# Performance work log

Measured on AMD Instinct MI355X. Metric: run time of the kernel, lower is better.

The kernel has to match this reference:

```python
import jax, jax.numpy as jnp
import numpy as np

B, L, D = 8, 8192, 256
H = 4 * D
EPS_LN = 1e-5
EPS_RELU = 1e-6
MIN_A, MAX_A, OFFSET = 0, 3, 3


def setup_inputs() -> dict:
    key = jax.random.key(0)
    ks = jax.random.split(key, 6)
    def n(k, shape, s=0.02):
        return jax.random.normal(k, shape, jnp.float32) * s
    return {
        "x": jax.random.normal(ks[0], (B, L, D), jnp.float32),
        "g1": jnp.ones((D,), jnp.float32), "b1": jnp.zeros((D,), jnp.float32),
        "g2": jnp.ones((D,), jnp.float32), "b2": jnp.zeros((D,), jnp.float32),
        "filt_w": n(ks[1], (L, D)),
        "w1": n(ks[2], (D, H)), "bb1": jnp.zeros((H,), jnp.float32),
        "w2": n(ks[3], (H, D)), "bb2": jnp.zeros((D,), jnp.float32),
    }


def layernorm(x, g, b):
    m = jnp.mean(x, -1, keepdims=True)
    v = jnp.var(x, -1, keepdims=True)
    return (x - m) * jax.lax.rsqrt(v + EPS_LN) * g + b


def maxpool_same(x, w):
    # stride-1 max pool over the last (frequency) axis, SAME padding
    if w == 1:
        return x
    return jax.lax.reduce_window(x, -jnp.inf, jax.lax.max,
                                 (1, 1, w), (1, 1, 1), "SAME")


def spsd1d(xt):
    """SPSD1D: FFT-based multi-scale (alpha) max-pooling spectral filter.
    xt: (B, D, L). Keeps rfft bins that are local maxima at every scale
    2**alpha for alpha in [MIN_A, MAX_A]; the lowest OFFSET bins pass through.
    Returns filtered signal (B, D, L) and argmax-alpha holder (B, D, F)."""
    X = jnp.fft.rfft(xt, axis=-1)              # (B, D, F), F = L//2 + 1
    mag = jnp.abs(X)
    pooled = jnp.stack([maxpool_same(mag, 2 ** a)
                        for a in range(MIN_A, MAX_A + 1)], 0)  # (A, B, D, F)
    max_holder = jnp.argmax(pooled, axis=0)
    env = jnp.max(pooled, axis=0)
    keep = (mag >= env) | (jnp.arange(mag.shape[-1]) < OFFSET)
    Xf = jnp.where(keep, X, 0.0)
    out = jnp.fft.irfft(Xf, n=xt.shape[-1], axis=-1)
    return out, max_holder


def _block_forward(x, g1, b1, g2, b2, filt_w, w1, bb1, w2, bb2):
    # EpsilonReLU(LayerNorm(x))
    h = jax.nn.relu(layernorm(x, g1, b1)) + EPS_RELU      # (B, L, D)
    # GlobalSPSDFilter: spsd over sequence axis, then elementwise weight
    f, _max_holder = spsd1d(jnp.swapaxes(h, 1, 2))        # (B, D, L)
    x0 = jnp.swapaxes(f, 1, 2) * filt_w                   # (B, L, D)
    # MLP(LayerNorm(x0)); dropouts are identity in eval mode
    m = layernorm(x0, g2, b2)
    m = jax.nn.gelu(m @ w1 + bb1, approximate=False)
    x0 = m @ w2 + bb2
    return x + x0


def reference(x, g1, b1, g2, b2, filt_w, w1, bb1, w2, bb2):
    return _block_forward(x, g1, b1, g2, b2, filt_w, w1, bb1, w2, bb2)
```

## Files before the change

### kernel.cpp

```cpp
#include <hip/hip_runtime.h>
#include <hip/hip_bf16.h>

#define BSZ  8
#define LSEQ 8192
#define DDIM 256
#define HDIM 1024
#define MFFT 4096

typedef __bf16 bf16;
typedef __bf16 bf16x8 __attribute__((ext_vector_type(8)));
typedef __bf16 bf16x4 __attribute__((ext_vector_type(4)));
typedef float  f32x4  __attribute__((ext_vector_type(4)));

__device__ __forceinline__ void wave_reduce2(float& a, float& b) {
    #pragma unroll
    for (int off = 1; off < 64; off <<= 1) {
        a += __shfl_xor(a, off);
        b += __shfl_xor(b, off);
    }
}

__device__ __forceinline__ void gl_lds16(const void* g, void* l) {
    __builtin_amdgcn_global_load_lds(
        (const __attribute__((address_space(1))) unsigned int*)(unsigned long long)g,
        (__attribute__((address_space(3))) unsigned int*)(unsigned int)(unsigned long long)l,
        16, 0, 0);
}

__global__ __launch_bounds__(256) void k0_prep(const float* __restrict__ w1,
                                               const float* __restrict__ w2,
                                               bf16* __restrict__ w1t,
                                               bf16* __restrict__ w2ct,
                                               float2* __restrict__ tbl) {
    const int e = blockIdx.x * 256 + threadIdx.x;
    {
        const int h = e >> 8, d = e & 255;
        w1t[e] = (bf16)w1[d * HDIM + h];
    }
    {
        const int hh = e & 63, d = (e >> 6) & 255, c = e >> 14;
        w2ct[e] = (bf16)w2[(c * 64 + hh) * DDIM + d];
    }
    if (e <= 8184) {
        float ang;
        if (e < 3584) {
            const int f = e / 512 + 1, jj = e & 511;
            ang = -6.283185307179586f * (float)(f * jj) * (1.0f / 4096.0f);
        } else if (e < 4032) {
            const int t = e - 3584, f = t / 64 + 1, jj = t & 63;
            ang = -6.283185307179586f * (float)(f * jj) * (1.0f / 512.0f);
        } else if (e < 4088) {
            const int t = e - 4032, f = t / 8 + 1, jj = t & 7;
            ang = -6.283185307179586f * (float)(f * jj) * (1.0f / 64.0f);
        } else {
            const int k = e - 4088;
            ang = 3.14159265358979323846f * (float)k * (1.0f / 4096.0f);
        }
        tbl[e] = make_float2(cosf(ang), sinf(ang));
    }
}

__global__ __launch_bounds__(256) void k1_ln1_relu_T(const float* __restrict__ x,
                                                     const float* __restrict__ g1,
                                                     const float* __restrict__ b1,
                                                     float* __restrict__ ht) {
    __shared__ float tile[DDIM][33];
    const int tid  = threadIdx.x;
    const int wave = tid >> 6, lane = tid & 63;
    const int b  = blockIdx.x >> 8;
    const int l0 = (blockIdx.x & 255) << 5;
    const float4 g4 = *(const float4*)&g1[lane * 4];
    const float4 b4 = *(const float4*)&b1[lane * 4];
    for (int r8 = 0; r8 < 8; ++r8) {
        const int l = r8 * 4 + wave;
        const float4 v = *(const float4*)&x[(b * LSEQ + l0 + l) * DDIM + lane * 4];
        float s = v.x + v.y + v.z + v.w;
        float q = v.x * v.x + v.y * v.y + v.z * v.z + v.w * v.w;
        wave_reduce2(s, q);
        const float mean = s * (1.0f / 256.0f);
        const float var  = q * (1.0f / 256.0f) - mean * mean;
        const float rstd = rsqrtf(var + 1e-5f);
        const float vv[4] = {v.x, v.y, v.z, v.w};
        const float gg[4] = {g4.x, g4.y, g4.z, g4.w};
        const float bb[4] = {b4.x, b4.y, b4.z, b4.w};
        #pragma unroll
        for (int j = 0; j < 4; ++j) {
            float t = (vv[j] - mean) * rstd * gg[j] + bb[j];
            t = fmaxf(t, 0.0f) + 1e-6f;
            tile[lane * 4 + j][l] = t;
        }
    }
    __syncthreads();
    for (int i = tid; i < DDIM * 32; i += 256) {
        const int d = i >> 5, ll = i & 31;
        ht[(b * DDIM + d) * LSEQ + l0 + ll] = tile[d][ll];
    }
}

__device__ __forceinline__ int zs(int p) { return p ^ ((p >> 4) & 15); }
__device__ __forceinline__ float2 cmulf(float2 a, float2 b) {
    return make_float2(fmaf(a.x, b.x, -a.y * b.y), fmaf(a.x, b.y, a.y * b.x));
}
__device__ __forceinline__ float2 f2add(float2 a, float2 b) { return make_float2(a.x + b.x, a.y + b.y); }
__device__ __forceinline__ float2 f2sub(float2 a, float2 b) { return make_float2(a.x - b.x, a.y - b.y); }
#define CSQ2 0.70710678118654752440f

__device__ __forceinline__ void dft8(float2 a0, float2 a1, float2 a2, float2 a3,
                                     float2 a4, float2 a5, float2 a6, float2 a7,
                                     float2& y0, float2& y1, float2& y2, float2& y3,
                                     float2& y4, float2& y5, float2& y6, float2& y7) {
    const float2 s0 = f2add(a0, a4), s1 = f2add(a1, a5), s2 = f2add(a2, a6), s3 = f2add(a3, a7);
    const float2 d0 = f2sub(a0, a4), d1 = f2sub(a1, a5), d2 = f2sub(a2, a6), d3 = f2sub(a3, a7);
    const float2 d1t = make_float2(CSQ2 * (d1.x + d1.y), CSQ2 * (d1.y - d1.x));
    const float2 d2t = make_float2(d2.y, -d2.x);
    const float2 d3t = make_float2(CSQ2 * (d3.y - d3.x), -CSQ2 * (d3.x + d3.y));
    const float2 u0 = f2add(s0, s2), u1 = f2add(s1, s3);
    const float2 v0 = f2sub(s0, s2);
    const float2 sd = f2sub(s1, s3);
    const float2 v1 = make_float2(sd.y, -sd.x);
    const float2 e0 = f2add(d0, d2t), e1 = f2add(d1t, d3t);
    const float2 f0 = f2sub(d0, d2t);
    const float2 dd = f2sub(d1t, d3t);
    const float2 f1 = make_float2(dd.y, -dd.x);
    y0 = f2add(u0, u1); y4 = f2sub(u0, u1);
    y2 = f2add(v0, v1); y6 = f2sub(v0, v1);
    y1 = f2add(e0, e1); y5 = f2sub(e0, e1);
    y3 = f2add(f0, f1); y7 = f2sub(f0, f1);
}

template<int LQ, int TOFF>
__device__ __forceinline__ void stage8(float2* Z, const float2* __restrict__ tw, int tid) {
    const int q = 1 << LQ;
    const int j = tid & (q - 1);
    const int base = ((tid >> LQ) << (LQ + 3)) + j;
    const float2 a0 = Z[zs(base)],         a1 = Z[zs(base + q)];
    const float2 a2 = Z[zs(base + 2 * q)], a3 = Z[zs(base + 3 * q)];
    const float2 a4 = Z[zs(base + 4 * q)], a5 = Z[zs(base + 5 * q)];
    const float2 a6 = Z[zs(base + 6 * q)], a7 = Z[zs(base + 7 * q)];
    float2 y0, y1, y2, y3, y4, y5, y6, y7;
    dft8(a0, a1, a2, a3, a4, a5, a6, a7, y0, y1, y2, y3, y4, y5, y6, y7);
    y1 = cmulf(y1, tw[TOFF + j]);
    y2 = cmulf(y2, tw[TOFF + q + j]);
    y3 = cmulf(y3, tw[TOFF + 2 * q + j]);
    y4 = cmulf(y4, tw[TOFF + 3 * q + j]);
    y5 = cmulf(y5, tw[TOFF + 4 * q + j]);
    y6 = cmulf(y6, tw[TOFF + 5 * q + j]);
    y7 = cmulf(y7, tw[TOFF + 6 * q + j]);
    Z[zs(base)]         = y0;
    Z[zs(base + 4 * q)] = y1;
    Z[zs(base + 2 * q)] = y2;
    Z[zs(base + 6 * q)] = y3;
    Z[zs(base + q)]     = y4;
    Z[zs(base + 5 * q)] = y5;
    Z[zs(base + 3 * q)] = y6;
    Z[zs(base + 7 * q)] = y7;
    __syncthreads();
}

__device__ __forceinline__ void stage8_last(float2* Z, int tid) {
    const int base = tid << 3;
    const float2 a0 = Z[zs(base)],     a1 = Z[zs(base + 1)];
    const float2 a2 = Z[zs(base + 2)], a3 = Z[zs(base + 3)];
    const float2 a4 = Z[zs(base + 4)], a5 = Z[zs(base + 5)];
    const float2 a6 = Z[zs(base + 6)], a7 = Z[zs(base + 7)];
    __syncthreads();
    float2 y0, y1, y2, y3, y4, y5, y6, y7;
    dft8(a0, a1, a2, a3, a4, a5, a6, a7, y0, y1, y2, y3, y4, y5, y6, y7);
    const int r9 = (int)(__brev((unsigned)tid) >> 23);
    Z[zs(r9)]        = y0;
    Z[zs(512 + r9)]  = y1;
    Z[zs(1024 + r9)] = y2;
    Z[zs(1536 + r9)] = y3;
    Z[zs(2048 + r9)] = y4;
    Z[zs(2560 + r9)] = y5;
    Z[zs(3072 + r9)] = y6;
    Z[zs(3584 + r9)] = y7;
    __syncthreads();
}

__device__ __forceinline__ void fft4096(float2* Z, const float2* __restrict__ tw, int tid) {
    stage8<9, 0>(Z, tw, tid);
    stage8<6, 3584>(Z, tw, tid);
    stage8<3, 4032>(Z, tw, tid);
    stage8_last(Z, tid);
}

__global__ __launch_bounds__(512, 4) void k2_spsd(float* __restrict__ ht,
                                                  const float2* __restrict__ tw) {
    __shared__ float2 Z[MFFT];
    __shared__ float  mg[MFFT + 1];
    const int tid = threadIdx.x;
    float* row = ht + (size_t)blockIdx.x * LSEQ;
    const float2* U = tw + 4088;

    for (int m = tid; m < MFFT; m += 512)
        Z[zs(m)] = *(const float2*)&row[2 * m];
    __syncthreads();

    fft4096(Z, tw, tid);

    for (int k = tid; k <= MFFT; k += 512) {
        const int ka = k & (MFFT - 1);
        const int kb = (MFFT - k) & (MFFT - 1);
        const float2 A = Z[zs(ka)], Bc = Z[zs(kb)];
        const float zex = 0.5f * (A.x + Bc.x), zey = 0.5f * (A.y - Bc.y);
        const float zox = 0.5f * (A.y + Bc.y), zoy = -0.5f * (A.x - Bc.x);
        const float2 u = U[k];
        const float cs = u.x, sn = -u.y;
        const float xr = zex + zox * cs - zoy * sn;
        const float xi = zey + zox * sn + zoy * cs;
        mg[k] = sqrtf(xr * xr + xi * xi);
    }
    __syncthreads();

    for (int k = tid; k <= 2048; k += 512) {
        const int km = (MFFT - k) & (MFFT - 1);
        const float2 Pk = Z[zs(k)];
        const float2 Pm = Z[zs(km)];
        const float2 u = U[k];
        const float cs = u.x, sn = u.y;
        const float zex = 0.5f * (Pk.x + Pm.x), zey = 0.5f * (Pk.y - Pm.y);
        const float zox = 0.5f * (Pk.y + Pm.y), zoy = -0.5f * (Pk.x - Pm.x);
        float xkr = zex + zox * cs + zoy * sn;
        float xki = zey - zox * sn + zoy * cs;
        const float zex2 = 0.5f * (Pm.x + Pk.x), zey2 = 0.5f * (Pm.y - Pk.y);
        const float zox2 = 0.5f * (Pm.y + Pk.y), zoy2 = -0.5f * (Pm.x - Pk.x);
        float xmr = zex2 - zox2 * cs + zoy2 * sn;
        float xmi = zey2 - zox2 * sn - zoy2 * cs;
        const int jm = MFFT - k;
        bool keepk, keepm;
        {
            const int lo = (k - 3 < 0) ? 0 : k - 3;
            const int hi = (k + 4 > 4096) ? 4096 : k + 4;
            float mx = mg[k];
            for (int t2 = lo; t2 <= hi; ++t2) mx = fmaxf(mx, mg[t2]);
            keepk = (k < 3) || (mg[k] >= mx);
        }
        {
            const int hi = (jm + 4 > 4096) ? 4096 : jm + 4;
            float mx = mg[jm];
            for (int t2 = jm - 3; t2 <= hi; ++t2) mx = fmaxf(mx, mg[t2]);
            keepm = (mg[jm] >= mx);
        }
        if (!keepk) { xkr = 0.0f; xki = 0.0f; }
        if (!keepm) { xmr = 0.0f; xmi = 0.0f; }
        const float zpex = 0.5f * (xkr + xmr), zpey = 0.5f * (xki - xmi);
        const float dfx  = 0.5f * (xkr - xmr), dfy  = 0.5f * (xki + xmi);
        const float zpox = dfx * cs - dfy * sn, zpoy = dfx * sn + dfy * cs;
        const float2 zk = make_float2(zpex - zpoy, zpey + zpox);
        const float zex3 = 0.5f * (xmr + xkr), zey3 = 0.5f * (xmi - xki);
        const float df2x = 0.5f * (xmr - xkr), df2y = 0.5f * (xmi + xki);
        const float zo3x = -df2x * cs - df2y * sn, zo3y = df2x * sn - df2y * cs;
        const float2 zm = make_float2(zex3 - zo3y, zey3 + zo3x);
        Z[zs(k)] = make_float2(zk.x, -zk.y);
        if (k != 0 && k != 2048) Z[zs(MFFT - k)] = make_float2(zm.x, -zm.y);
    }
    __syncthreads();

    fft4096(Z, tw, tid);

    const float invM = 1.0f / (float)MFFT;
    for (int m = tid; m < MFFT; m += 512) {
        const float2 z = Z[zs(m)];
        *(float2*)&row[2 * m] = make_float2(z.x * invM, -z.y * invM);
    }
}

__global__ __launch_bounds__(256) void k3_filt_ln2(const float* __restrict__ ht,
                                                   const float* __restrict__ fw,
                                                   const float* __restrict__ g2,
                                                   const float* __restrict__ b2,
                                                   bf16* __restrict__ aln) {
    __shared__ float tile[DDIM][33];
    const int tid  = threadIdx.x;
    const int wave = tid >> 6, lane = tid & 63;
    const int b  = blockIdx.x >> 8;
    const int l0 = (blockIdx.x & 255) << 5;
    for (int i = tid; i < DDIM * 32; i += 256) {
        const int d = i >> 5, ll = i & 31;
        tile[d][ll] = ht[(b * DDIM + d) * LSEQ + l0 + ll];
    }
    __syncthreads();
    const float4 g4 = *(const float4*)&g2[lane * 4];
    const float4 bb4 = *(const float4*)&b2[lane * 4];
    for (int r8 = 0; r8 < 8; ++r8) {
        const int l = r8 * 4 + wave;
        const int gl = l0 + l;
        const float4 f4 = *(const float4*)&fw[gl * DDIM + lane * 4];
        float v[4];
        v[0] = tile[lane * 4 + 0][l] * f4.x;
        v[1] = tile[lane * 4 + 1][l] * f4.y;
        v[2] = tile[lane * 4 + 2][l] * f4.z;
        v[3] = tile[lane * 4 + 3][l] * f4.w;
        float s = v[0] + v[1] + v[2] + v[3];
        float q = v[0] * v[0] + v[1] * v[1] + v[2] * v[2] + v[3] * v[3];
        wave_reduce2(s, q);
        const float mean = s * (1.0f / 256.0f);
        const float var  = q * (1.0f / 256.0f) - mean * mean;
        const float rstd = rsqrtf(var + 1e-5f);
        const float gg[4] = {g4.x, g4.y, g4.z, g4.w};
        const float bb[4] = {bb4.x, bb4.y, bb4.z, bb4.w};
        bf16x4 o;
        #pragma unroll
        for (int j = 0; j < 4; ++j)
            o[j] = (bf16)((v[j] - mean) * rstd * gg[j] + bb[j]);
        *(bf16x4*)&aln[(b * LSEQ + gl) * DDIM + lane * 4] = o;
    }
}

#define LDS_W1 0
#define LDS_W2 32768
#define LDS_LM 65536
#define LDS_TOT 81920

__global__ __launch_bounds__(512, 2) void k4_mlp(const bf16* __restrict__ aln,
                                                 const bf16* __restrict__ w1t,
                                                 const bf16* __restrict__ w2ct,
                                                 const float* __restrict__ bb1,
                                                 const float* __restrict__ bb2,
                                                 const float* __restrict__ x,
                                                 float* __restrict__ out) {
    extern __shared__ char sm[];
    const int tid = threadIdx.x;
    const int lane = tid & 63, w = tid >> 6;
    const int rowLane = lane & 15, grp = lane >> 4;
    const int wm = w >> 1, wn = w & 1;
    const int row0 = blockIdx.x << 7;
    const int sw = (rowLane & 7) << 4;

    bf16x8 aF[2][8];
    #pragma unroll
    for (int fm = 0; fm < 2; ++fm) {
        const size_t rb = (size_t)(row0 + wm * 32 + fm * 16 + rowLane) * DDIM;
        #pragma unroll
        for (int ks = 0; ks < 8; ++ks)
            aF[fm][ks] = *(const bf16x8*)(aln + rb + ks * 32 + grp * 8);
    }
    {
        const char* g1 = (const char*)w1t;
        #pragma unroll
        for (int r = 0; r < 4; ++r) {
            const int o = r * 8192 + tid * 16;
            gl_lds16(g1 + (o ^ (((o >> 9) & 7) << 4)), sm + LDS_W1 + o);
        }
    }
    __syncthreads();

    f32x4 acc[2][8];
    #pragma unroll
    for (int i = 0; i < 2; ++i)
        #pragma unroll
        for (int j2 = 0; j2 < 8; ++j2) acc[i][j2] = (f32x4){0.f, 0.f, 0.f, 0.f};

    for (int c = 0; c < 16; ++c) {
        {
            const char* g2 = (const char*)(w2ct + (size_t)c * DDIM * 64);
            #pragma unroll
            for (int r = 0; r < 4; ++r) {
                const int o = r * 8192 + tid * 16;
                gl_lds16(g2 + (o ^ (((o >> 7) & 7) << 4)), sm + LDS_W2 + o);
            }
        }
        const float bias0 = bb1[c * 64 + wn * 32 + rowLane];
        const float bias1 = bb1[c * 64 + wn * 32 + 16 + rowLane];

        f32x4 p00 = {0.f,0.f,0.f,0.f}, p01 = p00, p10 = p00, p11 = p00;
        const int hc0 = wn * 32 + rowLane;
        #pragma unroll
        for (int ks = 0; ks < 8; ++ks) {
            const int kb = (ks * 64 + grp * 16) ^ sw;
            const bf16x8 b0 = *(const bf16x8*)(sm + LDS_W1 + hc0 * 512 + kb);
            const bf16x8 b1 = *(const bf16x8*)(sm + LDS_W1 + (hc0 + 16) * 512 + kb);
            p00 = __builtin_amdgcn_mfma_f32_16x16x32_bf16(aF[0][ks], b0, p00, 0, 0, 0);
            p10 = __builtin_amdgcn_mfma_f32_16x16x32_bf16(aF[1][ks], b0, p10, 0, 0, 0);
            p01 = __builtin_amdgcn_mfma_f32_16x16x32_bf16(aF[0][ks], b1, p01, 0, 0, 0);
            p11 = __builtin_amdgcn_mfma_f32_16x16x32_bf16(aF[1][ks], b1, p11, 0, 0, 0);
        }
        #pragma unroll
        for (int fm = 0; fm < 2; ++fm)
        #pragma unroll
        for (int fn = 0; fn < 2; ++fn) {
            const f32x4 pv = fm ? (fn ? p11 : p10) : (fn ? p01 : p00);
            const int pcol2 = (wn * 32 + fn * 16 + rowLane) * 2;
            const float bias = fn ? bias1 : bias0;
            #pragma unroll
            for (int j = 0; j < 4; ++j) {
                const int prow = wm * 32 + fm * 16 + grp * 4 + j;
                const float v = pv[j] + bias;
                const float ge = 0.5f * v * (1.0f + erff(v * 0.70710678118654752f));
                *(bf16*)(sm + LDS_LM + prow * 128 + (pcol2 ^ ((prow & 7) << 4))) = (bf16)ge;
            }
        }
        __syncthreads();
        if (c < 15) {
            const char* g1 = (const char*)(w1t + (size_t)(c + 1) * 64 * DDIM);
            #pragma unroll
            for (int r = 0; r < 4; ++r) {
                const int o = r * 8192 + tid * 16;
                gl_lds16(g1 + (o ^ (((o >> 9) & 7) << 4)), sm + LDS_W1 + o);
            }
        }
        const int ar0 = wm * 32 + rowLane;
        #pragma unroll
        for (int kk = 0; kk < 2; ++kk) {
            const int kb = (kk * 64 + grp * 16) ^ sw;
            const bf16x8 a0 = *(const bf16x8*)(sm + LDS_LM + ar0 * 128 + kb);
            const bf16x8 a1 = *(const bf16x8*)(sm + LDS_LM + (ar0 + 16) * 128 + kb);
            #pragma unroll
            for (int fn = 0; fn < 8; ++fn) {
                const int dcol = wn * 128 + fn * 16 + rowLane;
                const bf16x8 bw = *(const bf16x8*)(sm + LDS_W2 + dcol * 128 + kb);
                acc[0][fn] = __builtin_amdgcn_mfma_f32_16x16x32_bf16(a0, bw, acc[0][fn], 0, 0, 0);
                acc[1][fn] = __builtin_amdgcn_mfma_f32_16x16x32_bf16(a1, bw, acc[1][fn], 0, 0, 0);
            }
        }
        __syncthreads();
    }
    #pragma unroll
    for (int fn = 0; fn < 8; ++fn) {
        const int dcol = wn * 128 + fn * 16 + rowLane;
        const float b2v = bb2[dcol];
        #pragma unroll
        for (int fm = 0; fm < 2; ++fm)
        #pragma unroll
        for (int j = 0; j < 4; ++j) {
            const int orow = row0 + wm * 32 + fm * 16 + grp * 4 + j;
            const int gi = orow * DDIM + dcol;
            out[gi] = acc[fm][fn][j] + b2v + x[gi];
        }
    }
}

extern "C" void kernel_launch(void* const* d_in, const int* in_sizes, int n_in,
                              void* d_out, int out_size, void* d_ws, size_t ws_size,
                              hipStream_t stream) {
    (void)in_sizes; (void)n_in; (void)out_size; (void)ws_size;
    const float* x   = (const float*)d_in[0];
    const float* g1  = (const float*)d_in[1];
    const float* b1  = (const float*)d_in[2];
    const float* g2  = (const float*)d_in[3];
    const float* b2  = (const float*)d_in[4];
    const float* fw  = (const float*)d_in[5];
    const float* w1  = (const float*)d_in[6];
    const float* bb1 = (const float*)d_in[7];
    const float* w2  = (const float*)d_in[8];
    const float* bb2 = (const float*)d_in[9];
    float* out = (float*)d_out;
    char*  ws  = (char*)d_ws;

    bf16*   aln  = (bf16*)ws;
    bf16*   w1t  = (bf16*)(ws + (size_t)33554432);
    bf16*   w2ct = (bf16*)(ws + (size_t)34078720);
    float2* tbl  = (float2*)(ws + (size_t)34603008);
    float* ht = out;

    k0_prep<<<dim3(1024), dim3(256), 0, stream>>>(w1, w2, w1t, w2ct, tbl);
    k1_ln1_relu_T<<<dim3(2048), dim3(256), 0, stream>>>(x, g1, b1, ht);
    k2_spsd<<<dim3(2048), dim3(512), 0, stream>>>(ht, tbl);
    k3_filt_ln2<<<dim3(2048), dim3(256), 0, stream>>>(ht, fw, g2, b2, aln);
    k4_mlp<<<dim3(512), dim3(512), LDS_TOT, stream>>>(aln, w1t, w2ct, bb1, bb2, x, out);
}
```

Baseline: 256.9 us.

## Pre-pack MLP weights in MFMA fragment order and halve hidden chunk size

The prep kernel now writes W1 and W2 in bf16 laid out in MFMA fragment order, so the MLP kernel can copy weights into LDS contiguously and read them without XOR swizzling. The hidden-dimension chunk shrinks from 64 to 32, which halves LDS use to 40 KB per block and allows more blocks per CU. The cost is twice as many loop iterations, and so twice as many barriers and more per-chunk overhead, with fewer MFMAs issued between each sync.

New measurement: 259.1 us. Within noise of the previous version (+0.8%).

```diff
diff --git a/kernel.cpp b/kernel.cpp
--- a/kernel.cpp
+++ b/kernel.cpp
@@ -29,17 +29,19 @@
 
 __global__ __launch_bounds__(256) void k0_prep(const float* __restrict__ w1,
                                                const float* __restrict__ w2,
-                                               bf16* __restrict__ w1t,
-                                               bf16* __restrict__ w2ct,
+                                               bf16* __restrict__ w1k,
+                                               bf16* __restrict__ w2k,
                                                float2* __restrict__ tbl) {
     const int e = blockIdx.x * 256 + threadIdx.x;
     {
-        const int h = e >> 8, d = e & 255;
-        w1t[e] = (bf16)w1[d * HDIM + h];
+        const int c = e >> 13, r = e & 8191;
+        const int ks = r >> 10, grp = (r >> 8) & 3, hh = (r >> 3) & 31, j = r & 7;
+        w1k[e] = (bf16)w1[(ks * 32 + grp * 8 + j) * HDIM + c * 32 + hh];
     }
     {
-        const int hh = e & 63, d = (e >> 6) & 255, c = e >> 14;
-        w2ct[e] = (bf16)w2[(c * 64 + hh) * DDIM + d];
+        const int c = e >> 13, r = e & 8191;
+        const int grp = r >> 11, d = (r >> 3) & 255, j = r & 7;
+        w2k[e] = (bf16)w2[(c * 32 + grp * 8 + j) * DDIM + d];
     }
     if (e <= 8184) {
         float ang;
@@ -309,13 +311,13 @@
 }
 
 #define LDS_W1 0
-#define LDS_W2 32768
-#define LDS_LM 65536
-#define LDS_TOT 81920
+#define LDS_W2 16384
+#define LDS_LM 32768
+#define LDS_TOT 40960
 
 __global__ __launch_bounds__(512, 2) void k4_mlp(const bf16* __restrict__ aln,
-                                                 const bf16* __restrict__ w1t,
-                                                 const bf16* __restrict__ w2ct,
+                                                 const bf16* __restrict__ w1k,
+                                                 const bf16* __restrict__ w2k,
                                                  const float* __restrict__ bb1,
                                                  const float* __restrict__ bb2,
                                                  const float* __restrict__ x,
@@ -326,7 +328,6 @@
     const int rowLane = lane & 15, grp = lane >> 4;
     const int wm = w >> 1, wn = w & 1;
     const int row0 = blockIdx.x << 7;
-    const int sw = (rowLane & 7) << 4;
 
     bf16x8 aF[2][8];
     #pragma unroll
@@ -337,12 +338,9 @@
             aF[fm][ks] = *(const bf16x8*)(aln + rb + ks * 32 + grp * 8);
     }
     {
-        const char* g1 = (const char*)w1t;
-        #pragma unroll
-        for (int r = 0; r < 4; ++r) {
-            const int o = r * 8192 + tid * 16;
-            gl_lds16(g1 + (o ^ (((o >> 9) & 7) << 4)), sm + LDS_W1 + o);
-        }
+        const char* g1 = (const char*)w1k;
+        gl_lds16(g1 + tid * 16, sm + LDS_W1 + tid * 16);
+        gl_lds16(g1 + 8192 + tid * 16, sm + LDS_W1 + 8192 + tid * 16);
     }
     __syncthreads();
 
@@ -352,67 +350,50 @@
         #pragma unroll
         for (int j2 = 0; j2 < 8; ++j2) acc[i][j2] = (f32x4){0.f, 0.f, 0.f, 0.f};
 
-    for (int c = 0; c < 16; ++c) {
+    for (int c = 0; c < 32; ++c) {
         {
-            const char* g2 = (const char*)(w2ct + (size_t)c * DDIM * 64);
-            #pragma unroll
-            for (int r = 0; r < 4; ++r) {
-                const int o = r * 8192 + tid * 16;
-                gl_lds16(g2 + (o ^ (((o >> 7) & 7) << 4)), sm + LDS_W2 + o);
-            }
-        }
-        const float bias0 = bb1[c * 64 + wn * 32 + rowLane];
-        const float bias1 = bb1[c * 64 + wn * 32 + 16 + rowLane];
-
-        f32x4 p00 = {0.f,0.f,0.f,0.f}, p01 = p00, p10 = p00, p11 = p00;
-        const int hc0 = wn * 32 + rowLane;
+            const char* g2 = (const char*)(w2k + (size_t)c * 8192);
+            gl_lds16(g2 + tid * 16, sm + LDS_W2 + tid * 16);
+            gl_lds16(g2 + 8192 + tid * 16, sm + LDS_W2 + 8192 + tid * 16);
+        }
+        const int hc = wn * 16 + rowLane;
+        const float bias = bb1[c * 32 + hc];
+
+        f32x4 p0 = {0.f, 0.f, 0.f, 0.f}, p1 = p0;
         #pragma unroll
         for (int ks = 0; ks < 8; ++ks) {
-            const int kb = (ks * 64 + grp * 16) ^ sw;
-            const bf16x8 b0 = *(const bf16x8*)(sm + LDS_W1 + hc0 * 512 + kb);
-            const bf16x8 b1 = *(const bf16x8*)(sm + LDS_W1 + (hc0 + 16) * 512 + kb);
-            p00 = __builtin_amdgcn_mfma_f32_16x16x32_bf16(aF[0][ks], b0, p00, 0, 0, 0);
-            p10 = __builtin_amdgcn_mfma_f32_16x16x32_bf16(aF[1][ks], b0, p10, 0, 0, 0);
-            p01 = __builtin_amdgcn_mfma_f32_16x16x32_bf16(aF[0][ks], b1, p01, 0, 0, 0);
-            p11 = __builtin_amdgcn_mfma_f32_16x16x32_bf16(aF[1][ks], b1, p11, 0, 0, 0);
-        }
-        #pragma unroll
-        for (int fm = 0; fm < 2; ++fm)
-        #pragma unroll
-        for (int fn = 0; fn < 2; ++fn) {
-            const f32x4 pv = fm ? (fn ? p11 : p10) : (fn ? p01 : p00);
-            const int pcol2 = (wn * 32 + fn * 16 + rowLane) * 2;
-            const float bias = fn ? bias1 : bias0;
+            const bf16x8 bF = *(const bf16x8*)(sm + LDS_W1 + ks * 2048 + grp * 512 + hc * 16);
+            p0 = __builtin_amdgcn_mfma_f32_16x16x32_bf16(aF[0][ks], bF, p0, 0, 0, 0);
+            p1 = __builtin_amdgcn_mfma_f32_16x16x32_bf16(aF[1][ks], bF, p1, 0, 0, 0);
+        }
+        const int kg = wn * 2 + (rowLane >> 3);
+        const int cb = (rowLane & 7) * 2;
+        #pragma unroll
+        for (int fm = 0; fm < 2; ++fm) {
+            const f32x4 pv = fm ? p1 : p0;
             #pragma unroll
             for (int j = 0; j < 4; ++j) {
                 const int prow = wm * 32 + fm * 16 + grp * 4 + j;
                 const float v = pv[j] + bias;
                 const float ge = 0.5f * v * (1.0f + erff(v * 0.70710678118654752f));
-                *(bf16*)(sm + LDS_LM + prow * 128 + (pcol2 ^ ((prow & 7) << 4))) = (bf16)ge;
+                *(bf16*)(sm + LDS_LM + kg * 2048 + prow * 16 + cb) = (bf16)ge;
             }
         }
         __syncthreads();
-        if (c < 15) {
-            const char* g1 = (const char*)(w1t + (size_t)(c + 1) * 64 * DDIM);
-            #pragma unroll
-            for (int r = 0; r < 4; ++r) {
-                const int o = r * 8192 + tid * 16;
-                gl_lds16(g1 + (o ^ (((o >> 9) & 7) << 4)), sm + LDS_W1 + o);
-            }
-        }
-        const int ar0 = wm * 32 + rowLane;
-        #pragma unroll
-        for (int kk = 0; kk < 2; ++kk) {
-            const int kb = (kk * 64 + grp * 16) ^ sw;
-            const bf16x8 a0 = *(const bf16x8*)(sm + LDS_LM + ar0 * 128 + kb);
-            const bf16x8 a1 = *(const bf16x8*)(sm + LDS_LM + (ar0 + 16) * 128 + kb);
-            #pragma unroll
-            for (int fn = 0; fn < 8; ++fn) {
-                const int dcol = wn * 128 + fn * 16 + rowLane;
-                const bf16x8 bw = *(const bf16x8*)(sm + LDS_W2 + dcol * 128 + kb);
-                acc[0][fn] = __builtin_amdgcn_mfma_f32_16x16x32_bf16(a0, bw, acc[0][fn], 0, 0, 0);
-                acc[1][fn] = __builtin_amdgcn_mfma_f32_16x16x32_bf16(a1, bw, acc[1][fn], 0, 0, 0);
-            }
+        if (c < 31) {
+            const char* g1 = (const char*)(w1k + (size_t)(c + 1) * 8192);
+            gl_lds16(g1 + tid * 16, sm + LDS_W1 + tid * 16);
+            gl_lds16(g1 + 8192 + tid * 16, sm + LDS_W1 + 8192 + tid * 16);
+        }
+        const int ar = wm * 32 + rowLane;
+        const bf16x8 a0 = *(const bf16x8*)(sm + LDS_LM + grp * 2048 + ar * 16);
+        const bf16x8 a1 = *(const bf16x8*)(sm + LDS_LM + grp * 2048 + (ar + 16) * 16);
+        #pragma unroll
+        for (int fn = 0; fn < 8; ++fn) {
+            const int dcol = wn * 128 + fn * 16 + rowLane;
+            const bf16x8 bw = *(const bf16x8*)(sm + LDS_W2 + grp * 4096 + dcol * 16);
+            acc[0][fn] = __builtin_amdgcn_mfma_f32_16x16x32_bf16(a0, bw, acc[0][fn], 0, 0, 0);
+            acc[1][fn] = __builtin_amdgcn_mfma_f32_16x16x32_bf16(a1, bw, acc[1][fn], 0, 0, 0);
         }
         __syncthreads();
     }
@@ -448,15 +429,15 @@
     float* out = (float*)d_out;
     char*  ws  = (char*)d_ws;
 
-    bf16*   aln  = (bf16*)ws;
-    bf16*   w1t  = (bf16*)(ws + (size_t)33554432);
-    bf16*   w2ct = (bf16*)(ws + (size_t)34078720);
-    float2* tbl  = (float2*)(ws + (size_t)34603008);
+    bf16*   aln = (bf16*)ws;
+    bf16*   w1k = (bf16*)(ws + (size_t)33554432);
+    bf16*   w2k = (bf16*)(ws + (size_t)34078720);
+    float2* tbl = (float2*)(ws + (size_t)34603008);
     float* ht = out;
 
-    k0_prep<<<dim3(1024), dim3(256), 0, stream>>>(w1, w2, w1t, w2ct, tbl);
+    k0_prep<<<dim3(1024), dim3(256), 0, stream>>>(w1, w2, w1k, w2k, tbl);
     k1_ln1_relu_T<<<dim3(2048), dim3(256), 0, stream>>>(x, g1, b1, ht);
     k2_spsd<<<dim3(2048), dim3(512), 0, stream>>>(ht, tbl);
     k3_filt_ln2<<<dim3(2048), dim3(256), 0, stream>>>(ht, fw, g2, b2, aln);
-    k4_mlp<<<dim3(512), dim3(512), LDS_TOT, stream>>>(aln, w1t, w2ct, bb1, bb2, x, out);
-}
+    k4_mlp<<<dim3(512), dim3(512), LDS_TOT, stream>>>(aln, w1k, w2k, bb1, bb2, x, out);
+}
```
